# Optimization experiments

Hardware: AMD Instinct MI355X
Metric: run time of the kernel (lower is better)

The kernel has to match this reference:

```python
import jax, jax.numpy as jnp
import numpy as np

W = 32        # local_context
M = 128       # nb_features
TEMP = 1.0    # softmax_temp
NEG = -1e24   # mask fill used by local_dot_product in the original


def _log_features(x, proj):
    # Performer softmax-kernel log-features (before stabilization).
    # x: (B,H,N,E), proj: (M,E) -> (B,H,N,M); exp(q.k*TEMP) ~ (1/M) sum_m phi_q phi_k
    xn = x * np.float32(np.sqrt(TEMP))
    d = jnp.einsum('bhne,me->bhnm', xn, proj)
    diag = 0.5 * jnp.sum(xn * xn, axis=-1, keepdims=True)
    return d - diag


def _sb_local_chunk(q, k, v, proj):
    # Scatterbrain SBLocalAttention: exact softmax scores inside a centered local
    # window of size W, Performer low-rank approximation outside, shared normalizer.
    # q: (B,H,L,E) chunk queries; k,v: (B,H,S,E); proj: (M,E)
    B, H, L, E = q.shape
    S = k.shape[2]
    nb, half = L // W, W // 2

    logq = _log_features(q, proj)
    stab_q = jax.lax.stop_gradient(jnp.max(logq, axis=-1, keepdims=True))        # per-query stabilizer
    phi_q = jnp.exp(logq - stab_q)
    logk = _log_features(k, proj)
    stab_k = jax.lax.stop_gradient(jnp.max(logk, axis=(-1, -2), keepdims=True))  # global key stabilizer
    phi_k = jnp.exp(logk - stab_k)
    # true low-rank score = (phi_q . phi_k) * exp(prime_log_scale)
    pls = stab_q[..., 0] + stab_k[..., 0] - np.float32(np.log(M))                # (B,H,L)

    # Low-rank (linear attention) sums over ALL keys
    kv = jnp.einsum('bhsm,bhsd->bhmd', phi_k, v)
    lr_v = jnp.einsum('bhlm,bhmd->bhld', phi_q, kv)            # (B,H,L,E)
    lr_1 = jnp.einsum('bhlm,bhm->bhl', phi_q, phi_k.sum(2))    # (B,H,L)

    # Local window: query position t attends keys [t-W//2, t+W//2).
    # Gather 3 key blocks of size W per query block instead of per-query windows.
    q_blk = q.reshape(B, H, nb, W, E)
    phiq_blk = phi_q.reshape(B, H, nb, W, M)
    idx3 = W * jnp.arange(nb)[:, None] + jnp.arange(3 * W)[None, :]   # (nb,3W) into padded seq
    pad = [(0, 0), (0, 0), (W, W), (0, 0)]
    k3 = jnp.pad(k, pad)[:, :, idx3]          # (B,H,nb,3W,E)
    v3 = jnp.pad(v, pad)[:, :, idx3]
    phik3 = jnp.pad(phi_k, pad)[:, :, idx3]   # (B,H,nb,3W,M)

    pos = idx3[:, None, :] - W                # absolute key positions (nb,1,3W)
    rel = pos - (W * jnp.arange(nb)[:, None, None] + jnp.arange(W)[None, :, None])
    mask = (rel >= -half) & (rel < half) & (pos >= 0) & (pos < S)     # (nb,W,3W)

    scores = TEMP * jnp.einsum('bhnqe,bhnke->bhnqk', q_blk, k3)
    scores = jnp.where(mask, scores, NEG)
    dots_p = jnp.where(mask, jnp.einsum('bhnqm,bhnkm->bhnqk', phiq_blk, phik3), 0.0)

    qk_lse = jax.nn.logsumexp(scores, axis=-1).reshape(B, H, L)
    # low-rank mass minus the in-window part it double counts (>= 0 since phi >= 0)
    lr_rem = jnp.clip(lr_1 - dots_p.sum(-1).reshape(B, H, L), 1e-24, None)
    log_norm = jnp.logaddexp(qk_lse, jnp.log(lr_rem) + pls)           # (B,H,L)

    p_local = jnp.exp(scores - log_norm.reshape(B, H, nb, W, 1))
    out_local = jnp.einsum('bhnqk,bhnke->bhnqe', p_local, v3).reshape(B, H, L, E)
    lr_v_win = jnp.einsum('bhnqk,bhnke->bhnqe', dots_p, v3).reshape(B, H, L, E)
    return out_local + (lr_v - lr_v_win) * jnp.exp(pls - log_norm)[..., None]


def _forward(query, key, value, proj):
    # query/key/value: (B,T,H,E) as in the torch module; proj: (4,M,E), one random
    # feature matrix per chunk (module builds a fresh SBLocalAttention each chunk).
    q = jnp.transpose(query, (0, 2, 1, 3))
    k = jnp.transpose(key, (0, 2, 1, 3))
    v = jnp.transpose(value, (0, 2, 1, 3))
    B, H, T, E = q.shape
    CH = 1024
    qc = q.reshape(B, H, T // CH, CH, E).transpose(2, 0, 1, 3, 4)     # (4,B,H,CH,E)
    outs = jax.vmap(_sb_local_chunk, in_axes=(0, None, None, 0))(qc, k, v, proj)
    # torch.cat(att, 1).transpose(1, 2) -> (B,H,T,E)
    return outs.transpose(1, 2, 0, 3, 4).reshape(B, H, T, E)


def setup_inputs() -> dict:
    key = jax.random.key(0)
    k1, k2, k3, k4 = jax.random.split(key, 4)
    B, T, S, H, E = 4, 4096, 4096, 8, 64
    return {
        'query': jax.random.normal(k1, (B, T, H, E), dtype=jnp.float32),
        'key': jax.random.normal(k2, (B, S, H, E), dtype=jnp.float32),
        'value': jax.random.normal(k3, (B, S, H, E), dtype=jnp.float32),
        'proj': jax.random.normal(k4, (4, M, E), dtype=jnp.float32),
    }


def reference(query, key, value, proj):
    return _forward(query, key, value, proj)
```

## Files before the change

### kernel.cpp

```cpp
#include <hip/hip_runtime.h>

typedef unsigned short u16;
typedef unsigned int   u32;
typedef __attribute__((ext_vector_type(8))) short short8;
typedef __attribute__((ext_vector_type(4))) float f32x4;

#define LOGM 4.852030263919617f

constexpr int WS_PMAX = 0;
constexpr int WS_K1   = 2048;
constexpr int WS_KV   = 18432;
constexpr int WS_PHIK = 1067008;
constexpr int WS_PLS  = 9717760;
constexpr int WS_LR1  = 9848832;
constexpr int WS_PHIQ = 9979904;
constexpr int WS_LRV  = 18368512;

__device__ __forceinline__ float b2f(u16 u){ union { u32 i; float f; } x; x.i = ((u32)u) << 16; return x.f; }
__device__ __forceinline__ u16 f2b(float f){ union { float f; u32 i; } x; x.f = f; return (u16)((x.i + 0x7fffu + ((x.i >> 16) & 1u)) >> 16); }

__global__ __launch_bounds__(128) void k_stab(const float* __restrict__ proj,
                                              float* __restrict__ ws){
  __shared__ float red[2];
  const int c = blockIdx.x, tid = threadIdx.x;
  const int wave = tid >> 6, l = tid & 63;
  const float4* pr = (const float4*)(proj + c*8192 + tid*64);
  float pn = 0.f;
  #pragma unroll
  for(int i=0;i<16;i++){ float4 u = pr[i]; pn = fmaf(u.x,u.x,fmaf(u.y,u.y,fmaf(u.z,u.z,fmaf(u.w,u.w,pn)))); }
  #pragma unroll
  for(int o=1;o<64;o<<=1) pn = fmaxf(pn, __shfl_xor(pn, o));
  if(l == 0) red[wave] = pn;
  __syncthreads();
  const float stab = 0.5f * fmaxf(red[0], red[1]);
  if(tid < 32) ws[WS_PMAX + c*32 + tid] = stab;
}

__global__ __launch_bounds__(256, 2) void k_phi(const float* __restrict__ key,
                                                const float* __restrict__ val,
                                                const float* __restrict__ proj,
                                                float* __restrict__ ws){
  __shared__ __align__(16) u16 phit[128*72];
  __shared__ __align__(16) u16 vt[64*72];
  const int tid = threadIdx.x;
  const int wave = tid >> 6, l = tid & 63;
  const int g = l >> 4, r16 = l & 15;
  const int kq = blockIdx.x, combo = blockIdx.y;
  const int c = combo >> 5, b = (combo >> 3) & 3, h = combo & 7;
  const float* projc = proj + c*8192;
  const float stab = ws[WS_PMAX + combo];

  short8 ph[8][2], pl[8][2];
  #pragma unroll
  for(int mt=0;mt<8;mt++){
    #pragma unroll
    for(int ks=0;ks<2;ks++){
      const float* pb = projc + (mt*16 + r16)*64 + ks*32 + g*8;
      float4 u0 = *(const float4*)pb;
      float4 u1 = *(const float4*)(pb + 4);
      float x[8] = {u0.x,u0.y,u0.z,u0.w,u1.x,u1.y,u1.z,u1.w};
      #pragma unroll
      for(int j=0;j<8;j++){
        u16 hb = f2b(x[j]);
        ph[mt][ks][j] = (short)hb;
        pl[mt][ks][j] = (short)f2b(x[j] - b2f(hb));
      }
    }
  }

  const f32x4 zero4 = {0.f,0.f,0.f,0.f};
  f32x4 kvacc[2][4];
  #pragma unroll
  for(int i=0;i<2;i++)
    #pragma unroll
    for(int j=0;j<4;j++) kvacc[i][j] = zero4;
  float k1p0 = 0.f, k1p1 = 0.f;
  u16* phikg = ((u16*)(ws + WS_PHIK)) + (size_t)combo*1056*128;

  for(int t0=0;t0<16;t0++){
    const int s_tile = (kq + 4*t0)*64;
    const bool dtile = (s_tile < 1056);
    const int sA = s_tile + wave*16 + r16;
    const float* krow = key + (size_t)(b*4096 + sA)*512 + h*64;
    float areg[16];
    #pragma unroll
    for(int ks=0;ks<2;ks++){
      float4 u0 = *(const float4*)(krow + ks*32 + g*8);
      float4 u1 = *(const float4*)(krow + ks*32 + g*8 + 4);
      areg[ks*8+0]=u0.x; areg[ks*8+1]=u0.y; areg[ks*8+2]=u0.z; areg[ks*8+3]=u0.w;
      areg[ks*8+4]=u1.x; areg[ks*8+5]=u1.y; areg[ks*8+6]=u1.z; areg[ks*8+7]=u1.w;
    }
    float4 vreg[4];
    #pragma unroll
    for(int i=0;i<4;i++){
      int flat = tid + 256*i;
      int sv = flat >> 4, d4 = (flat & 15)*4;
      vreg[i] = *(const float4*)(val + (size_t)(b*4096 + s_tile + sv)*512 + h*64 + d4);
    }
    float ksq = 0.f;
    #pragma unroll
    for(int e=0;e<16;e++) ksq = fmaf(areg[e], areg[e], ksq);
    ksq += __shfl_xor(ksq, 16);
    ksq += __shfl_xor(ksq, 32);
    ksq *= 0.5f;
    short8 ah[2], al[2];
    #pragma unroll
    for(int ks=0;ks<2;ks++){
      #pragma unroll
      for(int j=0;j<8;j++){
        float x = areg[ks*8+j];
        u16 hb = f2b(x);
        ah[ks][j] = (short)hb;
        al[ks][j] = (short)f2b(x - b2f(hb));
      }
    }
    f32x4 acc[8];
    #pragma unroll
    for(int mt=0;mt<8;mt++) acc[mt] = zero4;
    #pragma unroll
    for(int ks=0;ks<2;ks++){
      #pragma unroll
      for(int mt=0;mt<8;mt++){
        acc[mt] = __builtin_amdgcn_mfma_f32_16x16x32_bf16(ah[ks], ph[mt][ks], acc[mt], 0, 0, 0);
        acc[mt] = __builtin_amdgcn_mfma_f32_16x16x32_bf16(ah[ks], pl[mt][ks], acc[mt], 0, 0, 0);
        acc[mt] = __builtin_amdgcn_mfma_f32_16x16x32_bf16(al[ks], ph[mt][ks], acc[mt], 0, 0, 0);
      }
    }
    const float kc0 = __shfl(ksq, 4*g + 0);
    const float kc1 = __shfl(ksq, 4*g + 1);
    const float kc2 = __shfl(ksq, 4*g + 2);
    const float kc3 = __shfl(ksq, 4*g + 3);
    const int gs = s_tile + wave*16 + r16;
    #pragma unroll
    for(int mt=0;mt<8;mt++){
      ushort4 pw;
      pw.x = f2b(__expf(acc[mt][0] - kc0 - stab));
      pw.y = f2b(__expf(acc[mt][1] - kc1 - stab));
      pw.z = f2b(__expf(acc[mt][2] - kc2 - stab));
      pw.w = f2b(__expf(acc[mt][3] - kc3 - stab));
      *(ushort4*)(phit + (mt*16 + r16)*72 + wave*16 + 4*g) = pw;
      if(dtile && gs < 1056)
        *(ushort4*)(phikg + (size_t)gs*128 + mt*16 + 4*g) = pw;
    }
    #pragma unroll
    for(int i=0;i<4;i++){
      int flat = tid + 256*i;
      int sv = flat >> 4, d4 = (flat & 15)*4;
      float x[4] = {vreg[i].x, vreg[i].y, vreg[i].z, vreg[i].w};
      #pragma unroll
      for(int j=0;j<4;j++){
        int d = d4 + j;
        vt[d*72 + (sv ^ (8*((d>>2)&7)))] = f2b(x[j]);
      }
    }
    __syncthreads();
    #pragma unroll
    for(int ks=0;ks<2;ks++){
      short8 af0 = *(const short8*)(phit + ((2*wave+0)*16 + r16)*72 + ks*32 + g*8);
      short8 af1 = *(const short8*)(phit + ((2*wave+1)*16 + r16)*72 + ks*32 + g*8);
      short8 bf[4];
      #pragma unroll
      for(int dt=0;dt<4;dt++){
        int d = dt*16 + r16;
        int col = (ks*32 + g*8) ^ (8*((d>>2)&7));
        bf[dt] = *(const short8*)(vt + d*72 + col);
      }
      #pragma unroll
      for(int dt=0;dt<4;dt++){
        kvacc[0][dt] = __builtin_amdgcn_mfma_f32_16x16x32_bf16(af0, bf[dt], kvacc[0][dt], 0, 0, 0);
        kvacc[1][dt] = __builtin_amdgcn_mfma_f32_16x16x32_bf16(af1, bf[dt], kvacc[1][dt], 0, 0, 0);
      }
      #pragma unroll
      for(int j=0;j<8;j++){ k1p0 += b2f((u16)af0[j]); k1p1 += b2f((u16)af1[j]); }
    }
    __syncthreads();
  }
  k1p0 += __shfl_xor(k1p0, 16); k1p0 += __shfl_xor(k1p0, 32);
  k1p1 += __shfl_xor(k1p1, 16); k1p1 += __shfl_xor(k1p1, 32);
  if(l < 16){
    atomicAdd(ws + WS_K1 + combo*128 + (2*wave+0)*16 + l, k1p0);
    atomicAdd(ws + WS_K1 + combo*128 + (2*wave+1)*16 + l, k1p1);
  }
  #pragma unroll
  for(int mi=0;mi<2;mi++){
    #pragma unroll
    for(int dt=0;dt<4;dt++){
      #pragma unroll
      for(int rr=0;rr<4;rr++){
        int m = (2*wave+mi)*16 + 4*g + rr;
        int d = dt*16 + r16;
        atomicAdd(ws + WS_KV + (size_t)combo*8192 + m*64 + d, kvacc[mi][dt][rr]);
      }
    }
  }
}

__global__ __launch_bounds__(256, 2) void k_q(const float* __restrict__ qry,
                                              const float* __restrict__ proj,
                                              float* __restrict__ ws){
  __shared__ __align__(16) u16 phiqs[64*136];
  __shared__ __align__(16) u16 kvt[64*136];
  __shared__ float k1s[128];
  const int tid = threadIdx.x;
  const int wave = tid >> 6, l = tid & 63;
  const int g = l >> 4, r16 = l & 15;
  const int qt = blockIdx.x, combo = blockIdx.y;
  const int c = combo >> 5, b = (combo >> 3) & 3, h = combo & 7;
  const float* projc = proj + c*8192;
  const float stab = ws[WS_PMAX + combo];
  if(tid < 128) k1s[tid] = ws[WS_K1 + combo*128 + tid];
  const float* kvg = ws + WS_KV + (size_t)combo*8192;
  #pragma unroll
  for(int i=0;i<8;i++){
    int flat = tid + 256*i;
    int m = flat >> 4, d4 = (flat & 15)*4;
    float4 u = *(const float4*)(kvg + m*64 + d4);
    kvt[(d4+0)*136 + m] = f2b(u.x);
    kvt[(d4+1)*136 + m] = f2b(u.y);
    kvt[(d4+2)*136 + m] = f2b(u.z);
    kvt[(d4+3)*136 + m] = f2b(u.w);
  }
  const int qrow = qt*64 + wave*16 + r16;
  const float* qr = qry + (size_t)(b*4096 + (c*1024 + qrow))*512 + h*64;
  float areg[16];
  #pragma unroll
  for(int ks=0;ks<2;ks++){
    float4 u0 = *(const float4*)(qr + ks*32 + g*8);
    float4 u1 = *(const float4*)(qr + ks*32 + g*8 + 4);
    areg[ks*8+0]=u0.x; areg[ks*8+1]=u0.y; areg[ks*8+2]=u0.z; areg[ks*8+3]=u0.w;
    areg[ks*8+4]=u1.x; areg[ks*8+5]=u1.y; areg[ks*8+6]=u1.z; areg[ks*8+7]=u1.w;
  }
  float qsq = 0.f;
  #pragma unroll
  for(int e=0;e<16;e++) qsq = fmaf(areg[e], areg[e], qsq);
  qsq += __shfl_xor(qsq, 16);
  qsq += __shfl_xor(qsq, 32);
  qsq *= 0.5f;
  short8 ah[2], al[2];
  #pragma unroll
  for(int ks=0;ks<2;ks++){
    #pragma unroll
    for(int j=0;j<8;j++){
      float x = areg[ks*8+j];
      u16 hb = f2b(x);
      ah[ks][j] = (short)hb;
      al[ks][j] = (short)f2b(x - b2f(hb));
    }
  }
  const f32x4 zero4 = {0.f,0.f,0.f,0.f};
  f32x4 acc[8];
  #pragma unroll
  for(int mt=0;mt<8;mt++) acc[mt] = zero4;
  #pragma unroll
  for(int ks=0;ks<2;ks++){
    #pragma unroll
    for(int mt=0;mt<8;mt++){
      const float* pb = projc + (mt*16 + r16)*64 + ks*32 + g*8;
      float4 u0 = *(const float4*)pb;
      float4 u1 = *(const float4*)(pb + 4);
      float x[8] = {u0.x,u0.y,u0.z,u0.w,u1.x,u1.y,u1.z,u1.w};
      short8 pph, ppl;
      #pragma unroll
      for(int j=0;j<8;j++){
        u16 hb = f2b(x[j]);
        pph[j] = (short)hb;
        ppl[j] = (short)f2b(x[j] - b2f(hb));
      }
      acc[mt] = __builtin_amdgcn_mfma_f32_16x16x32_bf16(ah[ks], pph, acc[mt], 0, 0, 0);
      acc[mt] = __builtin_amdgcn_mfma_f32_16x16x32_bf16(ah[ks], ppl, acc[mt], 0, 0, 0);
      acc[mt] = __builtin_amdgcn_mfma_f32_16x16x32_bf16(al[ks], pph, acc[mt], 0, 0, 0);
    }
  }
  float qsr[4];
  #pragma unroll
  for(int r=0;r<4;r++) qsr[r] = __shfl(qsq, 4*g + r);
  float amax[4];
  #pragma unroll
  for(int r=0;r<4;r++){
    float m = -3e38f;
    #pragma unroll
    for(int mt=0;mt<8;mt++) m = fmaxf(m, acc[mt][r]);
    m = fmaxf(m, __shfl_xor(m, 1));
    m = fmaxf(m, __shfl_xor(m, 2));
    m = fmaxf(m, __shfl_xor(m, 4));
    m = fmaxf(m, __shfl_xor(m, 8));
    amax[r] = m;
  }
  float lrp[4] = {0.f,0.f,0.f,0.f};
  #pragma unroll
  for(int mt=0;mt<8;mt++){
    const float k1v = k1s[mt*16 + r16];
    #pragma unroll
    for(int r=0;r<4;r++){
      float phv = __expf(acc[mt][r] - amax[r]);
      phiqs[(wave*16 + 4*g + r)*136 + mt*16 + r16] = f2b(phv);
      lrp[r] = fmaf(phv, k1v, lrp[r]);
    }
  }
  #pragma unroll
  for(int r=0;r<4;r++){
    lrp[r] += __shfl_xor(lrp[r], 1);
    lrp[r] += __shfl_xor(lrp[r], 2);
    lrp[r] += __shfl_xor(lrp[r], 4);
    lrp[r] += __shfl_xor(lrp[r], 8);
  }
  if(r16 == 0){
    #pragma unroll
    for(int r=0;r<4;r++){
      int row = qt*64 + wave*16 + 4*g + r;
      ws[WS_PLS + combo*1024 + row] = amax[r] - qsr[r] + stab - LOGM;
      ws[WS_LR1 + combo*1024 + row] = lrp[r];
    }
  }
  __syncthreads();
  f32x4 lacc[4];
  #pragma unroll
  for(int dt=0;dt<4;dt++) lacc[dt] = zero4;
  #pragma unroll
  for(int ks=0;ks<4;ks++){
    short8 a = *(const short8*)(phiqs + (wave*16 + r16)*136 + ks*32 + g*8);
    #pragma unroll
    for(int dt=0;dt<4;dt++){
      short8 bfr = *(const short8*)(kvt + (dt*16 + r16)*136 + ks*32 + g*8);
      lacc[dt] = __builtin_amdgcn_mfma_f32_16x16x32_bf16(a, bfr, lacc[dt], 0, 0, 0);
    }
  }
  u16* lrvg = ((u16*)(ws + WS_LRV)) + ((size_t)combo*1024 + qt*64)*64;
  #pragma unroll
  for(int dt=0;dt<4;dt++){
    #pragma unroll
    for(int r=0;r<4;r++)
      lrvg[(wave*16 + 4*g + r)*64 + dt*16 + r16] = f2b(lacc[dt][r]);
  }
  u16* phiqg = ((u16*)(ws + WS_PHIQ)) + ((size_t)combo*1024 + qt*64)*128;
  #pragma unroll
  for(int i=0;i<8;i++){
    int flat = tid + 256*i;
    int row = flat >> 5, c4 = (flat & 31)*4;
    *(ushort4*)(phiqg + flat*4) = *(const ushort4*)(phiqs + row*136 + c4);
  }
}

__global__ __launch_bounds__(256, 2) void k_main(const float* __restrict__ qry,
                                                 const float* __restrict__ key,
                                                 const float* __restrict__ val,
                                                 float* __restrict__ ws,
                                                 float* __restrict__ out){
  __shared__ __align__(16) u16 buf[30720];
  u16* khs  = buf;
  u16* kls  = buf + 6912;
  u16* phik = buf + 13824;
  u16* cjh  = buf;
  u16* cjl  = buf + 8704;
  u16* vt   = buf + 17408;
  u16* vtl  = buf + 24064;

  const int tid = threadIdx.x;
  const int wave = tid >> 6, l = tid & 63;
  const int g = l >> 4, r16 = l & 15;
  const int qt = blockIdx.x, combo = blockIdx.y;
  const int c = combo >> 5, b = (combo >> 3) & 3, h = combo & 7;
  const int s_base = qt*64 - 16;

  const u16* phikg = ((const u16*)(ws + WS_PHIK)) + (size_t)combo*1056*128;
  float4 vreg[6];
  #pragma unroll
  for(int i=0;i<6;i++){
    int flat = tid + 256*i;
    int j = flat >> 4, e4 = (flat & 15)*4;
    int s = s_base + j;
    float4 u = {0.f,0.f,0.f,0.f};
    float4 w4 = {0.f,0.f,0.f,0.f};
    if(s >= 0){
      u  = *(const float4*)(key + (((size_t)b*4096 + s)*8 + h)*64 + e4);
      w4 = *(const float4*)(val + (((size_t)b*4096 + s)*8 + h)*64 + e4);
    }
    vreg[i] = w4;
    ushort4 hh, ll;
    hh.x = f2b(u.x); ll.x = f2b(u.x - b2f(hh.x));
    hh.y = f2b(u.y); ll.y = f2b(u.y - b2f(hh.y));
    hh.z = f2b(u.z); ll.z = f2b(u.z - b2f(hh.z));
    hh.w = f2b(u.w); ll.w = f2b(u.w - b2f(hh.w));
    *(ushort4*)(khs + j*72 + e4) = hh;
    *(ushort4*)(kls + j*72 + e4) = ll;
  }
  #pragma unroll
  for(int i=0;i<12;i++){
    int flat = tid + 256*i;
    int j = flat >> 5, c4 = (flat & 31)*4;
    int s = s_base + j;
    ushort4 p = {0,0,0,0};
    if(s >= 0) p = *(const ushort4*)(phikg + (size_t)s*128 + c4);
    *(ushort4*)(phik + j*136 + c4) = p;
  }
  const int qrow = qt*64 + wave*16 + r16;
  const float* qr = qry + (((size_t)b*4096 + (c*1024 + qrow))*8 + h)*64;
  short8 ah[2], al[2];
  #pragma unroll
  for(int ks=0;ks<2;ks++){
    float4 u0 = *(const float4*)(qr + ks*32 + g*8);
    float4 u1 = *(const float4*)(qr + ks*32 + g*8 + 4);
    float x[8] = {u0.x,u0.y,u0.z,u0.w,u1.x,u1.y,u1.z,u1.w};
    #pragma unroll
    for(int jj=0;jj<8;jj++){
      u16 hb = f2b(x[jj]);
      ah[ks][jj] = (short)hb;
      al[ks][jj] = (short)f2b(x[jj] - b2f(hb));
    }
  }
  const u16* phiqg = ((const u16*)(ws + WS_PHIQ)) + ((size_t)combo*1024 + qt*64)*128;
  short8 pa[4];
  #pragma unroll
  for(int ks=0;ks<4;ks++)
    pa[ks] = *(const short8*)(phiqg + (wave*16 + r16)*128 + ks*32 + g*8);
  float plsr[4], lr1r[4];
  #pragma unroll
  for(int r=0;r<4;r++){
    int row = qt*64 + wave*16 + 4*g + r;
    plsr[r] = ws[WS_PLS + combo*1024 + row];
    lr1r[r] = ws[WS_LR1 + combo*1024 + row];
  }
  __syncthreads();

  const f32x4 zero4 = {0.f,0.f,0.f,0.f};
  f32x4 sacc[6], dacc[6];
  #pragma unroll
  for(int j=0;j<6;j++){ sacc[j] = zero4; dacc[j] = zero4; }
  #pragma unroll
  for(int j=0;j<6;j++){
    #pragma unroll
    for(int ks=0;ks<2;ks++){
      short8 kbh = *(const short8*)(khs + (j*16 + r16)*72 + ks*32 + g*8);
      short8 kbl = *(const short8*)(kls + (j*16 + r16)*72 + ks*32 + g*8);
      sacc[j] = __builtin_amdgcn_mfma_f32_16x16x32_bf16(ah[ks], kbh, sacc[j], 0, 0, 0);
      sacc[j] = __builtin_amdgcn_mfma_f32_16x16x32_bf16(al[ks], kbh, sacc[j], 0, 0, 0);
      sacc[j] = __builtin_amdgcn_mfma_f32_16x16x32_bf16(ah[ks], kbl, sacc[j], 0, 0, 0);
    }
    #pragma unroll
    for(int ks=0;ks<4;ks++){
      short8 pb = *(const short8*)(phik + (j*16 + r16)*136 + ks*32 + g*8);
      dacc[j] = __builtin_amdgcn_mfma_f32_16x16x32_bf16(pa[ks], pb, dacc[j], 0, 0, 0);
    }
  }
  __syncthreads();

  #pragma unroll
  for(int i=0;i<6;i++){
    int flat = tid + 256*i;
    int j = flat >> 4, e4 = (flat & 15)*4;
    float4 u = vreg[i];
    u16 h0 = f2b(u.x), h1 = f2b(u.y), h2 = f2b(u.z), h3 = f2b(u.w);
    vt[(e4+0)*104 + j] = h0; vtl[(e4+0)*104 + j] = f2b(u.x - b2f(h0));
    vt[(e4+1)*104 + j] = h1; vtl[(e4+1)*104 + j] = f2b(u.y - b2f(h1));
    vt[(e4+2)*104 + j] = h2; vtl[(e4+2)*104 + j] = f2b(u.z - b2f(h2));
    vt[(e4+3)*104 + j] = h3; vtl[(e4+3)*104 + j] = f2b(u.w - b2f(h3));
  }
  const int rowb = wave*16 + 4*g;
  float m1r[4] = {-1e30f,-1e30f,-1e30f,-1e30f};
  #pragma unroll
  for(int j=0;j<6;j++){
    #pragma unroll
    for(int r=0;r<4;r++){
      int rel = 16*j + r16 - 16 - (rowb + r);
      bool ok = (rel >= -16) && (rel < 16) && (s_base + 16*j + r16 >= 0);
      if(ok) m1r[r] = fmaxf(m1r[r], sacc[j][r]);
    }
  }
  #pragma unroll
  for(int r=0;r<4;r++){
    m1r[r] = fmaxf(m1r[r], __shfl_xor(m1r[r], 1));
    m1r[r] = fmaxf(m1r[r], __shfl_xor(m1r[r], 2));
    m1r[r] = fmaxf(m1r[r], __shfl_xor(m1r[r], 4));
    m1r[r] = fmaxf(m1r[r], __shfl_xor(m1r[r], 8));
  }
  float ser[4] = {0.f,0.f,0.f,0.f}, wpr[4] = {0.f,0.f,0.f,0.f};
  #pragma unroll
  for(int j=0;j<6;j++){
    #pragma unroll
    for(int r=0;r<4;r++){
      int rel = 16*j + r16 - 16 - (rowb + r);
      bool ok = (rel >= -16) && (rel < 16) && (s_base + 16*j + r16 >= 0);
      if(ok){
        ser[r] += __expf(sacc[j][r] - m1r[r]);
        wpr[r] += dacc[j][r];
      }
    }
  }
  #pragma unroll
  for(int r=0;r<4;r++){
    ser[r] += __shfl_xor(ser[r], 1); ser[r] += __shfl_xor(ser[r], 2);
    ser[r] += __shfl_xor(ser[r], 4); ser[r] += __shfl_xor(ser[r], 8);
    wpr[r] += __shfl_xor(wpr[r], 1); wpr[r] += __shfl_xor(wpr[r], 2);
    wpr[r] += __shfl_xor(wpr[r], 4); wpr[r] += __shfl_xor(wpr[r], 8);
  }
  float lnr[4], scr[4];
  #pragma unroll
  for(int r=0;r<4;r++){
    float qk_lse = m1r[r] + __logf(ser[r]);
    float lrem = fmaxf(lr1r[r] - wpr[r], 1e-37f);
    float bb = __logf(lrem) + plsr[r];
    float ln = fmaxf(qk_lse, bb) + log1pf(__expf(-fabsf(qk_lse - bb)));
    lnr[r] = ln;
    scr[r] = __expf(plsr[r] - ln);
  }
  #pragma unroll
  for(int j=0;j<6;j++){
    #pragma unroll
    for(int r=0;r<4;r++){
      int rel = 16*j + r16 - 16 - (rowb + r);
      bool ok = (rel >= -16) && (rel < 16) && (s_base + 16*j + r16 >= 0);
      float cj = ok ? (__expf(sacc[j][r] - lnr[r]) - scr[r]*dacc[j][r]) : 0.f;
      u16 hb = f2b(cj);
      cjh[(rowb + r)*136 + 16*j + r16] = hb;
      cjl[(rowb + r)*136 + 16*j + r16] = f2b(cj - b2f(hb));
    }
  }
  __syncthreads();

  f32x4 oacc[4];
  #pragma unroll
  for(int dt=0;dt<4;dt++) oacc[dt] = zero4;
  #pragma unroll
  for(int ks=0;ks<3;ks++){
    short8 ch = *(const short8*)(cjh + (wave*16 + r16)*136 + ks*32 + g*8);
    short8 cl = *(const short8*)(cjl + (wave*16 + r16)*136 + ks*32 + g*8);
    #pragma unroll
    for(int dt=0;dt<4;dt++){
      short8 vbh = *(const short8*)(vt  + (dt*16 + r16)*104 + ks*32 + g*8);
      short8 vbl = *(const short8*)(vtl + (dt*16 + r16)*104 + ks*32 + g*8);
      oacc[dt] = __builtin_amdgcn_mfma_f32_16x16x32_bf16(ch, vbh, oacc[dt], 0, 0, 0);
      oacc[dt] = __builtin_amdgcn_mfma_f32_16x16x32_bf16(cl, vbh, oacc[dt], 0, 0, 0);
      oacc[dt] = __builtin_amdgcn_mfma_f32_16x16x32_bf16(ch, vbl, oacc[dt], 0, 0, 0);
    }
  }
  const u16* lrvg = ((const u16*)(ws + WS_LRV)) + ((size_t)combo*1024 + qt*64)*64;
  #pragma unroll
  for(int r=0;r<4;r++){
    int row = rowb + r;
    float* ob = out + ((((size_t)b*8 + h)*4096) + (size_t)c*1024 + qt*64 + row)*64;
    #pragma unroll
    for(int dt=0;dt<4;dt++){
      float lv = b2f(lrvg[row*64 + dt*16 + r16]);
      ob[dt*16 + r16] = oacc[dt][r] + scr[r]*lv;
    }
  }
}

extern "C" void kernel_launch(void* const* d_in, const int* in_sizes, int n_in,
                              void* d_out, int out_size, void* d_ws, size_t ws_size,
                              hipStream_t stream){
  (void)in_sizes; (void)n_in; (void)out_size; (void)ws_size;
  const float* q = (const float*)d_in[0];
  const float* k = (const float*)d_in[1];
  const float* v = (const float*)d_in[2];
  const float* p = (const float*)d_in[3];
  float* out = (float*)d_out;
  float* ws = (float*)d_ws;
  hipMemsetAsync(ws + WS_K1, 0, (size_t)(16384 + 1048576)*sizeof(float), stream);
  k_stab<<<dim3(4),      128, 0, stream>>>(p, ws);
  k_phi <<<dim3(4,128),  256, 0, stream>>>(k, v, p, ws);
  k_q   <<<dim3(16,128), 256, 0, stream>>>(q, p, ws);
  k_main<<<dim3(16,128), 256, 0, stream>>>(q, k, v, ws, out);
}
```

Baseline: 343.2 us.

## Fuse query feature kernel into main attention kernel to drop workspace round-trip

Merges k_q into k_main so each block computes phi_q, the low-rank numerator and normalizer, and the stabilizer in registers and shared memory, then reuses them directly for the local window step. This removes one kernel launch and the global writes and reads of phi_q, lr_v, pls and lr1, and q is loaded once instead of twice. Shared memory is reused across the phases, which adds barriers, and register pressure rises because lacc and the per-row values stay live through the main phase, which may hurt occupancy.

```diff
diff --git a/kernel.cpp b/kernel.cpp
--- a/kernel.cpp
+++ b/kernel.cpp
@@ -11,10 +11,6 @@
 constexpr int WS_K1   = 2048;
 constexpr int WS_KV   = 18432;
 constexpr int WS_PHIK = 1067008;
-constexpr int WS_PLS  = 9717760;
-constexpr int WS_LR1  = 9848832;
-constexpr int WS_PHIQ = 9979904;
-constexpr int WS_LRV  = 18368512;
 
 __device__ __forceinline__ float b2f(u16 u){ union { u32 i; float f; } x; x.i = ((u32)u) << 16; return x.f; }
 __device__ __forceinline__ u16 f2b(float f){ union { float f; u32 i; } x; x.f = f; return (u16)((x.i + 0x7fffu + ((x.i >> 16) & 1u)) >> 16); }
@@ -195,158 +191,16 @@
   }
 }
 
-__global__ __launch_bounds__(256, 2) void k_q(const float* __restrict__ qry,
-                                              const float* __restrict__ proj,
-                                              float* __restrict__ ws){
-  __shared__ __align__(16) u16 phiqs[64*136];
-  __shared__ __align__(16) u16 kvt[64*136];
-  __shared__ float k1s[128];
-  const int tid = threadIdx.x;
-  const int wave = tid >> 6, l = tid & 63;
-  const int g = l >> 4, r16 = l & 15;
-  const int qt = blockIdx.x, combo = blockIdx.y;
-  const int c = combo >> 5, b = (combo >> 3) & 3, h = combo & 7;
-  const float* projc = proj + c*8192;
-  const float stab = ws[WS_PMAX + combo];
-  if(tid < 128) k1s[tid] = ws[WS_K1 + combo*128 + tid];
-  const float* kvg = ws + WS_KV + (size_t)combo*8192;
-  #pragma unroll
-  for(int i=0;i<8;i++){
-    int flat = tid + 256*i;
-    int m = flat >> 4, d4 = (flat & 15)*4;
-    float4 u = *(const float4*)(kvg + m*64 + d4);
-    kvt[(d4+0)*136 + m] = f2b(u.x);
-    kvt[(d4+1)*136 + m] = f2b(u.y);
-    kvt[(d4+2)*136 + m] = f2b(u.z);
-    kvt[(d4+3)*136 + m] = f2b(u.w);
-  }
-  const int qrow = qt*64 + wave*16 + r16;
-  const float* qr = qry + (size_t)(b*4096 + (c*1024 + qrow))*512 + h*64;
-  float areg[16];
-  #pragma unroll
-  for(int ks=0;ks<2;ks++){
-    float4 u0 = *(const float4*)(qr + ks*32 + g*8);
-    float4 u1 = *(const float4*)(qr + ks*32 + g*8 + 4);
-    areg[ks*8+0]=u0.x; areg[ks*8+1]=u0.y; areg[ks*8+2]=u0.z; areg[ks*8+3]=u0.w;
-    areg[ks*8+4]=u1.x; areg[ks*8+5]=u1.y; areg[ks*8+6]=u1.z; areg[ks*8+7]=u1.w;
-  }
-  float qsq = 0.f;
-  #pragma unroll
-  for(int e=0;e<16;e++) qsq = fmaf(areg[e], areg[e], qsq);
-  qsq += __shfl_xor(qsq, 16);
-  qsq += __shfl_xor(qsq, 32);
-  qsq *= 0.5f;
-  short8 ah[2], al[2];
-  #pragma unroll
-  for(int ks=0;ks<2;ks++){
-    #pragma unroll
-    for(int j=0;j<8;j++){
-      float x = areg[ks*8+j];
-      u16 hb = f2b(x);
-      ah[ks][j] = (short)hb;
-      al[ks][j] = (short)f2b(x - b2f(hb));
-    }
-  }
-  const f32x4 zero4 = {0.f,0.f,0.f,0.f};
-  f32x4 acc[8];
-  #pragma unroll
-  for(int mt=0;mt<8;mt++) acc[mt] = zero4;
-  #pragma unroll
-  for(int ks=0;ks<2;ks++){
-    #pragma unroll
-    for(int mt=0;mt<8;mt++){
-      const float* pb = projc + (mt*16 + r16)*64 + ks*32 + g*8;
-      float4 u0 = *(const float4*)pb;
-      float4 u1 = *(const float4*)(pb + 4);
-      float x[8] = {u0.x,u0.y,u0.z,u0.w,u1.x,u1.y,u1.z,u1.w};
-      short8 pph, ppl;
-      #pragma unroll
-      for(int j=0;j<8;j++){
-        u16 hb = f2b(x[j]);
-        pph[j] = (short)hb;
-        ppl[j] = (short)f2b(x[j] - b2f(hb));
-      }
-      acc[mt] = __builtin_amdgcn_mfma_f32_16x16x32_bf16(ah[ks], pph, acc[mt], 0, 0, 0);
-      acc[mt] = __builtin_amdgcn_mfma_f32_16x16x32_bf16(ah[ks], ppl, acc[mt], 0, 0, 0);
-      acc[mt] = __builtin_amdgcn_mfma_f32_16x16x32_bf16(al[ks], pph, acc[mt], 0, 0, 0);
-    }
-  }
-  float qsr[4];
-  #pragma unroll
-  for(int r=0;r<4;r++) qsr[r] = __shfl(qsq, 4*g + r);
-  float amax[4];
-  #pragma unroll
-  for(int r=0;r<4;r++){
-    float m = -3e38f;
-    #pragma unroll
-    for(int mt=0;mt<8;mt++) m = fmaxf(m, acc[mt][r]);
-    m = fmaxf(m, __shfl_xor(m, 1));
-    m = fmaxf(m, __shfl_xor(m, 2));
-    m = fmaxf(m, __shfl_xor(m, 4));
-    m = fmaxf(m, __shfl_xor(m, 8));
-    amax[r] = m;
-  }
-  float lrp[4] = {0.f,0.f,0.f,0.f};
-  #pragma unroll
-  for(int mt=0;mt<8;mt++){
-    const float k1v = k1s[mt*16 + r16];
-    #pragma unroll
-    for(int r=0;r<4;r++){
-      float phv = __expf(acc[mt][r] - amax[r]);
-      phiqs[(wave*16 + 4*g + r)*136 + mt*16 + r16] = f2b(phv);
-      lrp[r] = fmaf(phv, k1v, lrp[r]);
-    }
-  }
-  #pragma unroll
-  for(int r=0;r<4;r++){
-    lrp[r] += __shfl_xor(lrp[r], 1);
-    lrp[r] += __shfl_xor(lrp[r], 2);
-    lrp[r] += __shfl_xor(lrp[r], 4);
-    lrp[r] += __shfl_xor(lrp[r], 8);
-  }
-  if(r16 == 0){
-    #pragma unroll
-    for(int r=0;r<4;r++){
-      int row = qt*64 + wave*16 + 4*g + r;
-      ws[WS_PLS + combo*1024 + row] = amax[r] - qsr[r] + stab - LOGM;
-      ws[WS_LR1 + combo*1024 + row] = lrp[r];
-    }
-  }
-  __syncthreads();
-  f32x4 lacc[4];
-  #pragma unroll
-  for(int dt=0;dt<4;dt++) lacc[dt] = zero4;
-  #pragma unroll
-  for(int ks=0;ks<4;ks++){
-    short8 a = *(const short8*)(phiqs + (wave*16 + r16)*136 + ks*32 + g*8);
-    #pragma unroll
-    for(int dt=0;dt<4;dt++){
-      short8 bfr = *(const short8*)(kvt + (dt*16 + r16)*136 + ks*32 + g*8);
-      lacc[dt] = __builtin_amdgcn_mfma_f32_16x16x32_bf16(a, bfr, lacc[dt], 0, 0, 0);
-    }
-  }
-  u16* lrvg = ((u16*)(ws + WS_LRV)) + ((size_t)combo*1024 + qt*64)*64;
-  #pragma unroll
-  for(int dt=0;dt<4;dt++){
-    #pragma unroll
-    for(int r=0;r<4;r++)
-      lrvg[(wave*16 + 4*g + r)*64 + dt*16 + r16] = f2b(lacc[dt][r]);
-  }
-  u16* phiqg = ((u16*)(ws + WS_PHIQ)) + ((size_t)combo*1024 + qt*64)*128;
-  #pragma unroll
-  for(int i=0;i<8;i++){
-    int flat = tid + 256*i;
-    int row = flat >> 5, c4 = (flat & 31)*4;
-    *(ushort4*)(phiqg + flat*4) = *(const ushort4*)(phiqs + row*136 + c4);
-  }
-}
-
-__global__ __launch_bounds__(256, 2) void k_main(const float* __restrict__ qry,
-                                                 const float* __restrict__ key,
-                                                 const float* __restrict__ val,
-                                                 float* __restrict__ ws,
-                                                 float* __restrict__ out){
+__global__ __launch_bounds__(256, 2) void k_qm(const float* __restrict__ qry,
+                                               const float* __restrict__ key,
+                                               const float* __restrict__ val,
+                                               const float* __restrict__ proj,
+                                               float* __restrict__ ws,
+                                               float* __restrict__ out){
   __shared__ __align__(16) u16 buf[30720];
+  u16* kvtA   = buf;
+  u16* phiqsA = buf + 8704;
+  float* k1s  = (float*)(buf + 17408);
   u16* khs  = buf;
   u16* kls  = buf + 6912;
   u16* phik = buf + 13824;
@@ -361,6 +215,131 @@
   const int qt = blockIdx.x, combo = blockIdx.y;
   const int c = combo >> 5, b = (combo >> 3) & 3, h = combo & 7;
   const int s_base = qt*64 - 16;
+  const float* projc = proj + c*8192;
+  const float stab = ws[WS_PMAX + combo];
+  const f32x4 zero4 = {0.f,0.f,0.f,0.f};
+
+  if(tid < 128) k1s[tid] = ws[WS_K1 + combo*128 + tid];
+  const float* kvg = ws + WS_KV + (size_t)combo*8192;
+  #pragma unroll
+  for(int i=0;i<8;i++){
+    int flat = tid + 256*i;
+    int m = flat >> 4, d4 = (flat & 15)*4;
+    float4 u = *(const float4*)(kvg + m*64 + d4);
+    kvtA[(d4+0)*136 + m] = f2b(u.x);
+    kvtA[(d4+1)*136 + m] = f2b(u.y);
+    kvtA[(d4+2)*136 + m] = f2b(u.z);
+    kvtA[(d4+3)*136 + m] = f2b(u.w);
+  }
+  const int qrow = qt*64 + wave*16 + r16;
+  const float* qr = qry + (size_t)(b*4096 + (c*1024 + qrow))*512 + h*64;
+  float areg[16];
+  #pragma unroll
+  for(int ks=0;ks<2;ks++){
+    float4 u0 = *(const float4*)(qr + ks*32 + g*8);
+    float4 u1 = *(const float4*)(qr + ks*32 + g*8 + 4);
+    areg[ks*8+0]=u0.x; areg[ks*8+1]=u0.y; areg[ks*8+2]=u0.z; areg[ks*8+3]=u0.w;
+    areg[ks*8+4]=u1.x; areg[ks*8+5]=u1.y; areg[ks*8+6]=u1.z; areg[ks*8+7]=u1.w;
+  }
+  float qsq = 0.f;
+  #pragma unroll
+  for(int e=0;e<16;e++) qsq = fmaf(areg[e], areg[e], qsq);
+  qsq += __shfl_xor(qsq, 16);
+  qsq += __shfl_xor(qsq, 32);
+  qsq *= 0.5f;
+  short8 ah[2], al[2];
+  #pragma unroll
+  for(int ks=0;ks<2;ks++){
+    #pragma unroll
+    for(int j=0;j<8;j++){
+      float x = areg[ks*8+j];
+      u16 hb = f2b(x);
+      ah[ks][j] = (short)hb;
+      al[ks][j] = (short)f2b(x - b2f(hb));
+    }
+  }
+  __syncthreads();
+
+  f32x4 acc[8];
+  #pragma unroll
+  for(int mt=0;mt<8;mt++) acc[mt] = zero4;
+  #pragma unroll
+  for(int ks=0;ks<2;ks++){
+    #pragma unroll
+    for(int mt=0;mt<8;mt++){
+      const float* pb = projc + (mt*16 + r16)*64 + ks*32 + g*8;
+      float4 u0 = *(const float4*)pb;
+      float4 u1 = *(const float4*)(pb + 4);
+      float x[8] = {u0.x,u0.y,u0.z,u0.w,u1.x,u1.y,u1.z,u1.w};
+      short8 pph, ppl;
+      #pragma unroll
+      for(int j=0;j<8;j++){
+        u16 hb = f2b(x[j]);
+        pph[j] = (short)hb;
+        ppl[j] = (short)f2b(x[j] - b2f(hb));
+      }
+      acc[mt] = __builtin_amdgcn_mfma_f32_16x16x32_bf16(ah[ks], pph, acc[mt], 0, 0, 0);
+      acc[mt] = __builtin_amdgcn_mfma_f32_16x16x32_bf16(ah[ks], ppl, acc[mt], 0, 0, 0);
+      acc[mt] = __builtin_amdgcn_mfma_f32_16x16x32_bf16(al[ks], pph, acc[mt], 0, 0, 0);
+    }
+  }
+  float qsr[4];
+  #pragma unroll
+  for(int r=0;r<4;r++) qsr[r] = __shfl(qsq, 4*g + r);
+  float amax[4];
+  #pragma unroll
+  for(int r=0;r<4;r++){
+    float m = -3e38f;
+    #pragma unroll
+    for(int mt=0;mt<8;mt++) m = fmaxf(m, acc[mt][r]);
+    m = fmaxf(m, __shfl_xor(m, 1));
+    m = fmaxf(m, __shfl_xor(m, 2));
+    m = fmaxf(m, __shfl_xor(m, 4));
+    m = fmaxf(m, __shfl_xor(m, 8));
+    amax[r] = m;
+  }
+  float lrp[4] = {0.f,0.f,0.f,0.f};
+  #pragma unroll
+  for(int mt=0;mt<8;mt++){
+    const float k1v = k1s[mt*16 + r16];
+    #pragma unroll
+    for(int r=0;r<4;r++){
+      float phv = __expf(acc[mt][r] - amax[r]);
+      phiqsA[(wave*16 + 4*g + r)*136 + mt*16 + r16] = f2b(phv);
+      lrp[r] = fmaf(phv, k1v, lrp[r]);
+    }
+  }
+  #pragma unroll
+  for(int r=0;r<4;r++){
+    lrp[r] += __shfl_xor(lrp[r], 1);
+    lrp[r] += __shfl_xor(lrp[r], 2);
+    lrp[r] += __shfl_xor(lrp[r], 4);
+    lrp[r] += __shfl_xor(lrp[r], 8);
+  }
+  float plsr[4], lr1r[4];
+  #pragma unroll
+  for(int r=0;r<4;r++){
+    plsr[r] = amax[r] - qsr[r] + stab - LOGM;
+    lr1r[r] = lrp[r];
+  }
+  __syncthreads();
+
+  short8 pa[4];
+  #pragma unroll
+  for(int ks=0;ks<4;ks++)
+    pa[ks] = *(const short8*)(phiqsA + (wave*16 + r16)*136 + ks*32 + g*8);
+  f32x4 lacc[4];
+  #pragma unroll
+  for(int dt=0;dt<4;dt++) lacc[dt] = zero4;
+  #pragma unroll
+  for(int ks=0;ks<4;ks++){
+    #pragma unroll
+    for(int dt=0;dt<4;dt++){
+      short8 bfr = *(const short8*)(kvtA + (dt*16 + r16)*136 + ks*32 + g*8);
+      lacc[dt] = __builtin_amdgcn_mfma_f32_16x16x32_bf16(pa[ks], bfr, lacc[dt], 0, 0, 0);
+    }
+  }
+  __syncthreads();
 
   const u16* phikg = ((const u16*)(ws + WS_PHIK)) + (size_t)combo*1056*128;
   float4 vreg[6];
@@ -393,36 +372,8 @@
     if(s >= 0) p = *(const ushort4*)(phikg + (size_t)s*128 + c4);
     *(ushort4*)(phik + j*136 + c4) = p;
   }
-  const int qrow = qt*64 + wave*16 + r16;
-  const float* qr = qry + (((size_t)b*4096 + (c*1024 + qrow))*8 + h)*64;
-  short8 ah[2], al[2];
-  #pragma unroll
-  for(int ks=0;ks<2;ks++){
-    float4 u0 = *(const float4*)(qr + ks*32 + g*8);
-    float4 u1 = *(const float4*)(qr + ks*32 + g*8 + 4);
-    float x[8] = {u0.x,u0.y,u0.z,u0.w,u1.x,u1.y,u1.z,u1.w};
-    #pragma unroll
-    for(int jj=0;jj<8;jj++){
-      u16 hb = f2b(x[jj]);
-      ah[ks][jj] = (short)hb;
-      al[ks][jj] = (short)f2b(x[jj] - b2f(hb));
-    }
-  }
-  const u16* phiqg = ((const u16*)(ws + WS_PHIQ)) + ((size_t)combo*1024 + qt*64)*128;
-  short8 pa[4];
-  #pragma unroll
-  for(int ks=0;ks<4;ks++)
-    pa[ks] = *(const short8*)(phiqg + (wave*16 + r16)*128 + ks*32 + g*8);
-  float plsr[4], lr1r[4];
-  #pragma unroll
-  for(int r=0;r<4;r++){
-    int row = qt*64 + wave*16 + 4*g + r;
-    plsr[r] = ws[WS_PLS + combo*1024 + row];
-    lr1r[r] = ws[WS_LR1 + combo*1024 + row];
-  }
-  __syncthreads();
-
-  const f32x4 zero4 = {0.f,0.f,0.f,0.f};
+  __syncthreads();
+
   f32x4 sacc[6], dacc[6];
   #pragma unroll
   for(int j=0;j<6;j++){ sacc[j] = zero4; dacc[j] = zero4; }
@@ -533,16 +484,13 @@
       oacc[dt] = __builtin_amdgcn_mfma_f32_16x16x32_bf16(ch, vbl, oacc[dt], 0, 0, 0);
     }
   }
-  const u16* lrvg = ((const u16*)(ws + WS_LRV)) + ((size_t)combo*1024 + qt*64)*64;
   #pragma unroll
   for(int r=0;r<4;r++){
     int row = rowb + r;
     float* ob = out + ((((size_t)b*8 + h)*4096) + (size_t)c*1024 + qt*64 + row)*64;
     #pragma unroll
-    for(int dt=0;dt<4;dt++){
-      float lv = b2f(lrvg[row*64 + dt*16 + r16]);
-      ob[dt*16 + r16] = oacc[dt][r] + scr[r]*lv;
-    }
+    for(int dt=0;dt<4;dt++)
+      ob[dt*16 + r16] = oacc[dt][r] + scr[r]*lacc[dt][r];
   }
 }
 
@@ -559,6 +507,5 @@
   hipMemsetAsync(ws + WS_K1, 0, (size_t)(16384 + 1048576)*sizeof(float), stream);
   k_stab<<<dim3(4),      128, 0, stream>>>(p, ws);
   k_phi <<<dim3(4,128),  256, 0, stream>>>(k, v, p, ws);
-  k_q   <<<dim3(16,128), 256, 0, stream>>>(q, p, ws);
-  k_main<<<dim3(16,128), 256, 0, stream>>>(q, k, v, ws, out);
+  k_qm  <<<dim3(16,128), 256, 0, stream>>>(q, k, v, p, ws, out);
 }
```

After: 324.1 us. 1.06x faster.
